# Performance work log

Hardware: AMD Instinct MI355X
Metric: run time of the kernel (lower is better)

## Reference

```python
import jax, jax.numpy as jnp
import numpy as np

KS = 1                      # search radius -> (2*KS+1)^3 = 27 offsets
TEMP = 0.00005              # softmax temperature
COEFS = [0.003, 0.01, 0.03, 0.1, 0.3, 1.0]
H, W, D = 96, 80, 128


def gaussian_kernel3d(channels, sigma=0.5):
    # matches torch GaussianBlur3D: kernel_size = int(2*sigma*2+1) = 3 for sigma=0.5
    ksz = int(2.0 * sigma * 2 + 1)
    c = jnp.arange(ksz, dtype=jnp.float32)
    zz, yy, xx = jnp.meshgrid(c, c, c, indexing='ij')
    mean = (ksz - 1) / 2.0
    var = sigma ** 2
    g = (1.0 / (2.0 * np.pi * var) ** 1.5) * jnp.exp(
        -((zz - mean) ** 2 + (yy - mean) ** 2 + (xx - mean) ** 2) / (2.0 * var))
    g = g / g.sum()
    k = jnp.broadcast_to(g[None, None], (channels, 1, ksz, ksz, ksz))
    return k, ksz // 2


def blur3d(x, kernel, pad):
    # depthwise 3D conv (groups == channels), padding 'same'
    C = x.shape[1]
    return jax.lax.conv_general_dilated(
        x, kernel, window_strides=(1, 1, 1),
        padding=[(pad, pad)] * 3,
        dimension_numbers=('NCDHW', 'OIDHW', 'NCDHW'),
        feature_group_count=C)


def make_offsets(ks):
    n = 2 * ks + 1
    oz, oy, ox = np.meshgrid(np.arange(n) - ks, np.arange(n) - ks,
                             np.arange(n) - ks, indexing='ij')
    off = np.stack([oz.ravel(), oy.ravel(), ox.ravel()], 0).astype(np.float32)
    return jnp.asarray(off).reshape(1, 3, n ** 3, 1, 1, 1)


def cost_volume(src, tgt, ks):
    # -mean_c |src_shifted - tgt| for each of the (2ks+1)^3 offsets
    b, c, h, w, d = src.shape
    xp = jnp.pad(src, ((0, 0), (0, 0), (ks, ks), (ks, ks), (ks, ks)))
    vols = []
    for i in range(2 * ks + 1):
        for j in range(2 * ks + 1):
            for k in range(2 * ks + 1):
                corr = jnp.abs(xp[:, :, i:i + h, j:j + w, k:k + d] - tgt).mean(axis=1)
                vols.append(-corr)
    cv = jnp.stack(vols, axis=1)          # (b, 27, h, w, d)
    return cv[:, None]                    # (b, 1, 27, h, w, d)


def argmax_onehot(cv, temp):
    p = jax.nn.softmax(cv / temp, axis=2)
    return (p == p.max(axis=2, keepdims=True)).astype(cv.dtype)


def setup_inputs() -> dict:
    key = jax.random.key(0)
    k1, k2 = jax.random.split(key)
    source = jax.random.uniform(k1, (1, 1, H, W, D), dtype=jnp.float32)
    target = jax.random.uniform(k2, (1, 1, H, W, D), dtype=jnp.float32)
    return {"source": source, "target": target}


def reference(source, target):
    offsets = make_offsets(KS)                              # (1,3,27,1,1,1)
    n3 = (2 * KS + 1) ** 3
    k_ks, p_ks = gaussian_kernel3d(n3, sigma=0.5)           # 27-ch depthwise blur
    k_3, p_3 = gaussian_kernel3d(3, sigma=0.5)              # 3-ch flow blur

    cv = cost_volume(source, target, KS)                    # (b,1,27,h,w,d)

    cvb = cv[:, 0]
    for _ in range(3):
        cvb = blur3d(cvb, k_ks, p_ks)
    cv = cvb[:, None]

    oh = argmax_onehot(cv, TEMP)                            # (b,1,27,h,w,d)
    flow = (oh * offsets).sum(axis=2)                       # (b,3,h,w,d)
    for _ in range(3):
        flow = blur3d(flow, k_3, p_3)

    for coeff in COEFS:
        # coupling term: squared distance of current flow to each offset
        dist2 = ((flow[:, :, None] - offsets) ** 2).sum(axis=1)  # (b,27,h,w,d)
        coupled = cv - coeff * dist2[:, None]
        oh = argmax_onehot(coupled, TEMP)
        flow = (oh * offsets).sum(axis=2)
        for _ in range(3):
            flow = blur3d(flow, k_3, p_3)
    return flow
```

## Files before the change

### kernel.cpp

```cpp
#include <hip/hip_runtime.h>
#include <math.h>

#define HH 96
#define WW 80
#define DD 128
#define SLICE (WW * DD)
#define NVOX (HH * WW * DD)

struct W4d { double w0, w1, w2, w3; };
struct Raw { float4 t[3]; float4 s[3]; };

__device__ __forceinline__ float4 zf4() { return make_float4(0.f, 0.f, 0.f, 0.f); }

template <bool FUSED>
__global__ __launch_bounds__(256) void blur4_kernel(
    const float* __restrict__ in, const float* __restrict__ src,
    const float* __restrict__ tgt, float* __restrict__ out, int zslab, W4d w) {
  const int tid = threadIdx.x;
  const int lane = tid & 63;
  const int q = lane & 31;
  const int x0 = q << 2;
  const int y = blockIdx.x * 8 + ((tid >> 6) << 1) + (lane >> 5);
  const int c = blockIdx.z;
  const int z0 = blockIdx.y * zslab;
  const int z1 = min(z0 + zslab, HH);

  int oz = 0, oy = 0, ox = 0;
  if (FUSED) { oz = c / 9 - 1; oy = (c / 3) % 3 - 1; ox = c % 3 - 1; }
  const float* __restrict__ inc = FUSED ? (const float*)nullptr : (in + (size_t)c * NVOX);

  auto load_raw = [&](int zz, Raw& r) {
    #pragma unroll
    for (int dy = 0; dy < 3; ++dy) {
      int ry = y - 1 + dy;
      bool rv = ((unsigned)zz < (unsigned)HH) && ((unsigned)ry < (unsigned)WW);
      if (!FUSED) {
        r.t[dy] = rv ? *(const float4*)(inc + (size_t)zz * SLICE + ry * DD + x0) : zf4();
      } else {
        r.t[dy] = rv ? *(const float4*)(tgt + (size_t)zz * SLICE + ry * DD + x0) : zf4();
        int sz = zz + oz, sy = ry + oy;
        bool sv = rv && ((unsigned)sz < (unsigned)HH) && ((unsigned)sy < (unsigned)WW);
        r.s[dy] = sv ? *(const float4*)(src + (size_t)sz * SLICE + sy * DD + x0) : zf4();
      }
    }
  };

  auto finish = [&](const Raw& r, double* P, double* Q) {
    float cc[3][4], cl[3], cr[3];
    #pragma unroll
    for (int dy = 0; dy < 3; ++dy) {
      float4 v;
      if (!FUSED) {
        v = r.t[dy];
      } else {
        float4 s4 = r.s[dy];
        float sl = __shfl_up(s4.w, 1);
        float sr = __shfl_down(s4.x, 1);
        if (q == 0) sl = 0.f;
        if (q == 31) sr = 0.f;
        float4 sh;
        if (ox < 0)      sh = make_float4(sl, s4.x, s4.y, s4.z);
        else if (ox > 0) sh = make_float4(s4.y, s4.z, s4.w, sr);
        else             sh = s4;
        float4 t4 = r.t[dy];
        v.x = -fabsf(__fsub_rn(sh.x, t4.x));
        v.y = -fabsf(__fsub_rn(sh.y, t4.y));
        v.z = -fabsf(__fsub_rn(sh.z, t4.z));
        v.w = -fabsf(__fsub_rn(sh.w, t4.w));
      }
      float l = __shfl_up(v.w, 1);
      float rr = __shfl_down(v.x, 1);
      cc[dy][0] = v.x; cc[dy][1] = v.y; cc[dy][2] = v.z; cc[dy][3] = v.w;
      cl[dy] = (q == 0) ? 0.f : l;
      cr[dy] = (q == 31) ? 0.f : rr;
    }
    auto hs = [&](int row, int i) -> double {
      float a = (i == 0) ? cl[row] : cc[row][i - 1];
      float b = (i == 3) ? cr[row] : cc[row][i + 1];
      return (double)a + (double)b;
    };
    #pragma unroll
    for (int i = 0; i < 4; ++i) {
      double c2 = (double)cc[1][i];
      double f2 = hs(1, i) + ((double)cc[0][i] + (double)cc[2][i]);
      double e2 = hs(0, i) + hs(2, i);
      P[i] = (w.w0 * c2 + w.w1 * f2) + w.w2 * e2;
      Q[i] = (w.w1 * c2 + w.w2 * f2) + w.w3 * e2;
    }
  };

  Raw rA, rB, rC, rD;
  double PA[4], QA[4], PB[4], QB[4], PC[4], QC[4];
  load_raw(z0 - 1, rA);
  load_raw(z0, rB);
  load_raw(z0 + 1, rC);
  finish(rA, PA, QA);
  finish(rB, PB, QB);
  float* ob = out + (size_t)c * NVOX + y * DD + x0;
  for (int z = z0; z < z1; ++z) {
    load_raw(z + 2, rD);
    finish(rC, PC, QC);
    float4 o4;
    o4.x = (float)(PB[0] + (QA[0] + QC[0]));
    o4.y = (float)(PB[1] + (QA[1] + QC[1]));
    o4.z = (float)(PB[2] + (QA[2] + QC[2]));
    o4.w = (float)(PB[3] + (QA[3] + QC[3]));
    *(float4*)(ob + (size_t)z * SLICE) = o4;
    #pragma unroll
    for (int i = 0; i < 4; ++i) {
      PA[i] = PB[i]; QA[i] = QB[i];
      PB[i] = PC[i]; QB[i] = QC[i];
    }
    rC = rD;
  }
}

__global__ __launch_bounds__(256) void flow4_kernel(
    const float* __restrict__ cv, const float* __restrict__ fin,
    float coeff, int couple, float* __restrict__ fout) {
  const int t = blockIdx.x * blockDim.x + threadIdx.x;
  const size_t v = (size_t)t * 4;
  if (v >= (size_t)NVOX) return;
  float4 fz = zf4(), fy = zf4(), fx = zf4();
  if (couple) {
    fz = *(const float4*)(fin + v);
    fy = *(const float4*)(fin + (size_t)NVOX + v);
    fx = *(const float4*)(fin + 2 * (size_t)NVOX + v);
  }
  float best[4] = {-INFINITY, -INFINITY, -INFINITY, -INFINITY};
  float s0[4] = {0, 0, 0, 0}, s1[4] = {0, 0, 0, 0}, s2[4] = {0, 0, 0, 0};
  float fza[4] = {fz.x, fz.y, fz.z, fz.w};
  float fya[4] = {fy.x, fy.y, fy.z, fy.w};
  float fxa[4] = {fx.x, fx.y, fx.z, fx.w};
  #pragma unroll
  for (int o = 0; o < 27; ++o) {
    float4 c4 = *(const float4*)(cv + (size_t)o * NVOX + v);
    const float ozf = (float)(o / 9 - 1);
    const float oyf = (float)((o / 3) % 3 - 1);
    const float oxf = (float)(o % 3 - 1);
    float ca[4] = {c4.x, c4.y, c4.z, c4.w};
    #pragma unroll
    for (int i = 0; i < 4; ++i) {
      float cvv = ca[i];
      if (couple) {
        float dz = __fsub_rn(fza[i], ozf);
        float dy = __fsub_rn(fya[i], oyf);
        float dx = __fsub_rn(fxa[i], oxf);
        float d2 = __fadd_rn(__fadd_rn(__fmul_rn(dz, dz), __fmul_rn(dy, dy)),
                             __fmul_rn(dx, dx));
        cvv = __fsub_rn(cvv, __fmul_rn(coeff, d2));
      }
      float yv = __fdiv_rn(cvv, 5e-5f);
      bool gt = yv > best[i];
      bool eq = yv == best[i];
      best[i] = gt ? yv : best[i];
      s0[i] = gt ? ozf : (eq ? s0[i] + ozf : s0[i]);
      s1[i] = gt ? oyf : (eq ? s1[i] + oyf : s1[i]);
      s2[i] = gt ? oxf : (eq ? s2[i] + oxf : s2[i]);
    }
  }
  *(float4*)(fout + v) = make_float4(s0[0], s0[1], s0[2], s0[3]);
  *(float4*)(fout + (size_t)NVOX + v) = make_float4(s1[0], s1[1], s1[2], s1[3]);
  *(float4*)(fout + 2 * (size_t)NVOX + v) = make_float4(s2[0], s2[1], s2[2], s2[3]);
}

extern "C" void kernel_launch(void* const* d_in, const int* in_sizes, int n_in,
                              void* d_out, int out_size, void* d_ws, size_t ws_size,
                              hipStream_t stream) {
  const float* src = (const float*)d_in[0];
  const float* tgt = (const float*)d_in[1];
  float* out = (float*)d_out;

  float* cv1 = (float*)d_ws;
  float* cv2 = cv1 + (size_t)27 * NVOX;
  float* fa = cv2;
  float* fb = cv2 + (size_t)3 * NVOX;

  float wt[27];
  {
    volatile float factor = (float)(1.0 / pow(2.0 * M_PI * 0.25, 1.5));
    float g[27];
    int o = 0;
    for (int i = 0; i < 3; ++i)
      for (int j = 0; j < 3; ++j)
        for (int k = 0; k < 3; ++k) {
          int d2 = (i - 1) * (i - 1) + (j - 1) * (j - 1) + (k - 1) * (k - 1);
          volatile float e = (float)exp(-2.0 * (double)d2);
          volatile float gg = factor * e;
          g[o++] = gg;
        }
    volatile float r[8];
    for (int j = 0; j < 8; ++j) r[j] = g[j];
    for (int j = 0; j < 8; ++j) r[j] = r[j] + g[8 + j];
    for (int j = 0; j < 8; ++j) r[j] = r[j] + g[16 + j];
    volatile float t01 = r[0] + r[1];
    volatile float t23 = r[2] + r[3];
    volatile float t45 = r[4] + r[5];
    volatile float t67 = r[6] + r[7];
    volatile float h0 = t01 + t23;
    volatile float h1 = t45 + t67;
    volatile float s = h0 + h1;
    s = s + g[24];
    s = s + g[25];
    s = s + g[26];
    for (int t = 0; t < 27; ++t) {
      volatile float w = g[t] / s;
      wt[t] = w;
    }
  }
  W4d wd = {(double)wt[13], (double)wt[12], (double)wt[9], (double)wt[0]};

  dim3 blk(256);
  dim3 gBig(WW / 8, HH / 8, 27);
  dim3 gSm(WW / 8, HH / 3, 3);
  int fblocks = NVOX / 4 / 256;

  blur4_kernel<true><<<gBig, blk, 0, stream>>>(nullptr, src, tgt, cv1, 8, wd);
  blur4_kernel<false><<<gBig, blk, 0, stream>>>(cv1, nullptr, nullptr, cv2, 8, wd);
  blur4_kernel<false><<<gBig, blk, 0, stream>>>(cv2, nullptr, nullptr, cv1, 8, wd);
  flow4_kernel<<<fblocks, blk, 0, stream>>>(cv1, nullptr, 0.f, 0, fa);
  blur4_kernel<false><<<gSm, blk, 0, stream>>>(fa, nullptr, nullptr, fb, 3, wd);
  blur4_kernel<false><<<gSm, blk, 0, stream>>>(fb, nullptr, nullptr, fa, 3, wd);
  blur4_kernel<false><<<gSm, blk, 0, stream>>>(fa, nullptr, nullptr, fb, 3, wd);
  const float coefs[6] = {0.003f, 0.01f, 0.03f, 0.1f, 0.3f, 1.0f};
  for (int it = 0; it < 6; ++it) {
    flow4_kernel<<<fblocks, blk, 0, stream>>>(cv1, fb, coefs[it], 1, fa);
    blur4_kernel<false><<<gSm, blk, 0, stream>>>(fa, nullptr, nullptr, fb, 3, wd);
    blur4_kernel<false><<<gSm, blk, 0, stream>>>(fb, nullptr, nullptr, fa, 3, wd);
    float* dst = (it == 5) ? out : fb;
    blur4_kernel<false><<<gSm, blk, 0, stream>>>(fa, nullptr, nullptr, dst, 3, wd);
  }
}
```

Baseline: 557.8 us.

## Fuse the third flow blur into the coupled argmax kernel and restructure blur math

Folds the last of each group of three flow blurs into a new kernel that blurs the three flow channels for a z-slab in registers and then runs the 27-offset coupled argmax on them. This removes one launch and one write-then-read of the 3-channel flow field per iteration. The blur stencil is refactored to share top and bottom row sums and use fma, which may change double rounding slightly. In exchange, blur work is recomputed at the slab halos and register pressure rises.

```diff
diff --git a/kernel.cpp b/kernel.cpp
--- a/kernel.cpp
+++ b/kernel.cpp
@@ -11,6 +11,54 @@
 struct Raw { float4 t[3]; float4 s[3]; };
 
 __device__ __forceinline__ float4 zf4() { return make_float4(0.f, 0.f, 0.f, 0.f); }
+
+__device__ __forceinline__ void pq_rows(const float4 rows[3], int q, const W4d& w,
+                                        double P[4], double Q[4]) {
+  double d[3][6];
+  #pragma unroll
+  for (int r = 0; r < 3; ++r) {
+    float4 v = rows[r];
+    float l = __shfl_up(v.w, 1);
+    float rr = __shfl_down(v.x, 1);
+    if (q == 0) l = 0.f;
+    if (q == 31) rr = 0.f;
+    d[r][0] = (double)l;
+    d[r][1] = (double)v.x;
+    d[r][2] = (double)v.y;
+    d[r][3] = (double)v.z;
+    d[r][4] = (double)v.w;
+    d[r][5] = (double)rr;
+  }
+  double tb[6];
+  #pragma unroll
+  for (int j = 0; j < 6; ++j) tb[j] = d[0][j] + d[2][j];
+  #pragma unroll
+  for (int i = 0; i < 4; ++i) {
+    double c2 = d[1][i + 1];
+    double f2 = (d[1][i] + d[1][i + 2]) + tb[i + 1];
+    double e2 = tb[i] + tb[i + 2];
+    P[i] = fma(w.w0, c2, fma(w.w1, f2, w.w2 * e2));
+    Q[i] = fma(w.w1, c2, fma(w.w2, f2, w.w3 * e2));
+  }
+}
+
+__device__ __forceinline__ void cv_rows(const Raw& r, int q, int ox, float4 rows[3]) {
+  #pragma unroll
+  for (int dy = 0; dy < 3; ++dy) {
+    float4 s4 = r.s[dy];
+    float sl = __shfl_up(s4.w, 1);
+    float sr = __shfl_down(s4.x, 1);
+    if (q == 0) sl = 0.f;
+    if (q == 31) sr = 0.f;
+    float4 sh;
+    if (ox < 0)      sh = make_float4(sl, s4.x, s4.y, s4.z);
+    else if (ox > 0) sh = make_float4(s4.y, s4.z, s4.w, sr);
+    else             sh = s4;
+    float4 t4 = r.t[dy];
+    rows[dy] = make_float4(-fabsf(__fsub_rn(sh.x, t4.x)), -fabsf(__fsub_rn(sh.y, t4.y)),
+                           -fabsf(__fsub_rn(sh.z, t4.z)), -fabsf(__fsub_rn(sh.w, t4.w)));
+  }
+}
 
 template <bool FUSED>
 __global__ __launch_bounds__(256) void blur4_kernel(
@@ -45,93 +93,121 @@
     }
   };
 
-  auto finish = [&](const Raw& r, double* P, double* Q) {
-    float cc[3][4], cl[3], cr[3];
-    #pragma unroll
-    for (int dy = 0; dy < 3; ++dy) {
-      float4 v;
-      if (!FUSED) {
-        v = r.t[dy];
-      } else {
-        float4 s4 = r.s[dy];
-        float sl = __shfl_up(s4.w, 1);
-        float sr = __shfl_down(s4.x, 1);
-        if (q == 0) sl = 0.f;
-        if (q == 31) sr = 0.f;
-        float4 sh;
-        if (ox < 0)      sh = make_float4(sl, s4.x, s4.y, s4.z);
-        else if (ox > 0) sh = make_float4(s4.y, s4.z, s4.w, sr);
-        else             sh = s4;
-        float4 t4 = r.t[dy];
-        v.x = -fabsf(__fsub_rn(sh.x, t4.x));
-        v.y = -fabsf(__fsub_rn(sh.y, t4.y));
-        v.z = -fabsf(__fsub_rn(sh.z, t4.z));
-        v.w = -fabsf(__fsub_rn(sh.w, t4.w));
-      }
-      float l = __shfl_up(v.w, 1);
-      float rr = __shfl_down(v.x, 1);
-      cc[dy][0] = v.x; cc[dy][1] = v.y; cc[dy][2] = v.z; cc[dy][3] = v.w;
-      cl[dy] = (q == 0) ? 0.f : l;
-      cr[dy] = (q == 31) ? 0.f : rr;
-    }
-    auto hs = [&](int row, int i) -> double {
-      float a = (i == 0) ? cl[row] : cc[row][i - 1];
-      float b = (i == 3) ? cr[row] : cc[row][i + 1];
-      return (double)a + (double)b;
-    };
-    #pragma unroll
-    for (int i = 0; i < 4; ++i) {
-      double c2 = (double)cc[1][i];
-      double f2 = hs(1, i) + ((double)cc[0][i] + (double)cc[2][i]);
-      double e2 = hs(0, i) + hs(2, i);
-      P[i] = (w.w0 * c2 + w.w1 * f2) + w.w2 * e2;
-      Q[i] = (w.w1 * c2 + w.w2 * f2) + w.w3 * e2;
-    }
+  auto finishF = [&](const Raw& r, double P[4], double Q[4]) {
+    float4 rows[3];
+    if (FUSED) cv_rows(r, q, ox, rows);
+    else { rows[0] = r.t[0]; rows[1] = r.t[1]; rows[2] = r.t[2]; }
+    pq_rows(rows, q, w, P, Q);
   };
 
   Raw rA, rB, rC, rD;
-  double PA[4], QA[4], PB[4], QB[4], PC[4], QC[4];
   load_raw(z0 - 1, rA);
   load_raw(z0, rB);
   load_raw(z0 + 1, rC);
-  finish(rA, PA, QA);
-  finish(rB, PB, QB);
+  double Pd[4], Qm[4], Pc[4], Qc[4];
+  finishF(rA, Pd, Qm);
+  finishF(rB, Pc, Qc);
   float* ob = out + (size_t)c * NVOX + y * DD + x0;
   for (int z = z0; z < z1; ++z) {
     load_raw(z + 2, rD);
-    finish(rC, PC, QC);
+    double Pn[4], Qn[4];
+    finishF(rC, Pn, Qn);
     float4 o4;
-    o4.x = (float)(PB[0] + (QA[0] + QC[0]));
-    o4.y = (float)(PB[1] + (QA[1] + QC[1]));
-    o4.z = (float)(PB[2] + (QA[2] + QC[2]));
-    o4.w = (float)(PB[3] + (QA[3] + QC[3]));
+    o4.x = (float)(Pc[0] + (Qm[0] + Qn[0]));
+    o4.y = (float)(Pc[1] + (Qm[1] + Qn[1]));
+    o4.z = (float)(Pc[2] + (Qm[2] + Qn[2]));
+    o4.w = (float)(Pc[3] + (Qm[3] + Qn[3]));
     *(float4*)(ob + (size_t)z * SLICE) = o4;
     #pragma unroll
-    for (int i = 0; i < 4; ++i) {
-      PA[i] = PB[i]; QA[i] = QB[i];
-      PB[i] = PC[i]; QB[i] = QC[i];
-    }
+    for (int i = 0; i < 4; ++i) { Qm[i] = Qc[i]; Qc[i] = Qn[i]; Pc[i] = Pn[i]; }
     rC = rD;
   }
 }
 
+template <int ZSLAB>
+__global__ __launch_bounds__(256) void blur_flow_kernel(
+    const float* __restrict__ fin, const float* __restrict__ cvb,
+    float coeff, float* __restrict__ fout, W4d w) {
+  const int tid = threadIdx.x;
+  const int lane = tid & 63;
+  const int q = lane & 31;
+  const int x0 = q << 2;
+  const int y = blockIdx.x * 8 + ((tid >> 6) << 1) + (lane >> 5);
+  const int z0 = blockIdx.y * ZSLAB;
+
+  float bl[3][ZSLAB][4];
+  #pragma unroll
+  for (int c = 0; c < 3; ++c) {
+    const float* __restrict__ inc = fin + (size_t)c * NVOX;
+    auto load_t = [&](int zz, float4 t3[3]) {
+      #pragma unroll
+      for (int dy = 0; dy < 3; ++dy) {
+        int ry = y - 1 + dy;
+        bool rv = ((unsigned)zz < (unsigned)HH) && ((unsigned)ry < (unsigned)WW);
+        t3[dy] = rv ? *(const float4*)(inc + (size_t)zz * SLICE + ry * DD + x0) : zf4();
+      }
+    };
+    float4 rA[3], rB[3], rC[3], rD[3];
+    load_t(z0 - 1, rA);
+    load_t(z0, rB);
+    load_t(z0 + 1, rC);
+    double Pd[4], Qm[4], Pc[4], Qc[4];
+    pq_rows(rA, q, w, Pd, Qm);
+    pq_rows(rB, q, w, Pc, Qc);
+    #pragma unroll
+    for (int zi = 0; zi < ZSLAB; ++zi) {
+      load_t(z0 + zi + 2, rD);
+      double Pn[4], Qn[4];
+      pq_rows(rC, q, w, Pn, Qn);
+      #pragma unroll
+      for (int i = 0; i < 4; ++i) bl[c][zi][i] = (float)(Pc[i] + (Qm[i] + Qn[i]));
+      #pragma unroll
+      for (int i = 0; i < 4; ++i) { Qm[i] = Qc[i]; Qc[i] = Qn[i]; Pc[i] = Pn[i]; }
+      rC[0] = rD[0]; rC[1] = rD[1]; rC[2] = rD[2];
+    }
+  }
+  #pragma unroll
+  for (int zi = 0; zi < ZSLAB; ++zi) {
+    size_t v = (size_t)(z0 + zi) * SLICE + y * DD + x0;
+    float best[4] = {-INFINITY, -INFINITY, -INFINITY, -INFINITY};
+    float s0[4] = {0, 0, 0, 0}, s1[4] = {0, 0, 0, 0}, s2[4] = {0, 0, 0, 0};
+    #pragma unroll
+    for (int o = 0; o < 27; ++o) {
+      float4 c4 = *(const float4*)(cvb + (size_t)o * NVOX + v);
+      const float ozf = (float)(o / 9 - 1);
+      const float oyf = (float)((o / 3) % 3 - 1);
+      const float oxf = (float)(o % 3 - 1);
+      float ca[4] = {c4.x, c4.y, c4.z, c4.w};
+      #pragma unroll
+      for (int i = 0; i < 4; ++i) {
+        float dz = __fsub_rn(bl[0][zi][i], ozf);
+        float dy2 = __fsub_rn(bl[1][zi][i], oyf);
+        float dx = __fsub_rn(bl[2][zi][i], oxf);
+        float d2 = __fadd_rn(__fadd_rn(__fmul_rn(dz, dz), __fmul_rn(dy2, dy2)),
+                             __fmul_rn(dx, dx));
+        float cvv = __fsub_rn(ca[i], __fmul_rn(coeff, d2));
+        float yv = __fdiv_rn(cvv, 5e-5f);
+        bool gt = yv > best[i];
+        bool eq = yv == best[i];
+        best[i] = gt ? yv : best[i];
+        s0[i] = gt ? ozf : (eq ? s0[i] + ozf : s0[i]);
+        s1[i] = gt ? oyf : (eq ? s1[i] + oyf : s1[i]);
+        s2[i] = gt ? oxf : (eq ? s2[i] + oxf : s2[i]);
+      }
+    }
+    *(float4*)(fout + v) = make_float4(s0[0], s0[1], s0[2], s0[3]);
+    *(float4*)(fout + (size_t)NVOX + v) = make_float4(s1[0], s1[1], s1[2], s1[3]);
+    *(float4*)(fout + 2 * (size_t)NVOX + v) = make_float4(s2[0], s2[1], s2[2], s2[3]);
+  }
+}
+
 __global__ __launch_bounds__(256) void flow4_kernel(
-    const float* __restrict__ cv, const float* __restrict__ fin,
-    float coeff, int couple, float* __restrict__ fout) {
+    const float* __restrict__ cv, float* __restrict__ fout) {
   const int t = blockIdx.x * blockDim.x + threadIdx.x;
   const size_t v = (size_t)t * 4;
   if (v >= (size_t)NVOX) return;
-  float4 fz = zf4(), fy = zf4(), fx = zf4();
-  if (couple) {
-    fz = *(const float4*)(fin + v);
-    fy = *(const float4*)(fin + (size_t)NVOX + v);
-    fx = *(const float4*)(fin + 2 * (size_t)NVOX + v);
-  }
   float best[4] = {-INFINITY, -INFINITY, -INFINITY, -INFINITY};
   float s0[4] = {0, 0, 0, 0}, s1[4] = {0, 0, 0, 0}, s2[4] = {0, 0, 0, 0};
-  float fza[4] = {fz.x, fz.y, fz.z, fz.w};
-  float fya[4] = {fy.x, fy.y, fy.z, fy.w};
-  float fxa[4] = {fx.x, fx.y, fx.z, fx.w};
   #pragma unroll
   for (int o = 0; o < 27; ++o) {
     float4 c4 = *(const float4*)(cv + (size_t)o * NVOX + v);
@@ -141,16 +217,7 @@
     float ca[4] = {c4.x, c4.y, c4.z, c4.w};
     #pragma unroll
     for (int i = 0; i < 4; ++i) {
-      float cvv = ca[i];
-      if (couple) {
-        float dz = __fsub_rn(fza[i], ozf);
-        float dy = __fsub_rn(fya[i], oyf);
-        float dx = __fsub_rn(fxa[i], oxf);
-        float d2 = __fadd_rn(__fadd_rn(__fmul_rn(dz, dz), __fmul_rn(dy, dy)),
-                             __fmul_rn(dx, dx));
-        cvv = __fsub_rn(cvv, __fmul_rn(coeff, d2));
-      }
-      float yv = __fdiv_rn(cvv, 5e-5f);
+      float yv = __fdiv_rn(ca[i], 5e-5f);
       bool gt = yv > best[i];
       bool eq = yv == best[i];
       best[i] = gt ? yv : best[i];
@@ -213,21 +280,28 @@
   dim3 blk(256);
   dim3 gBig(WW / 8, HH / 8, 27);
   dim3 gSm(WW / 8, HH / 3, 3);
+  dim3 gBF(WW / 8, HH / 2);
   int fblocks = NVOX / 4 / 256;
 
   blur4_kernel<true><<<gBig, blk, 0, stream>>>(nullptr, src, tgt, cv1, 8, wd);
   blur4_kernel<false><<<gBig, blk, 0, stream>>>(cv1, nullptr, nullptr, cv2, 8, wd);
   blur4_kernel<false><<<gBig, blk, 0, stream>>>(cv2, nullptr, nullptr, cv1, 8, wd);
-  flow4_kernel<<<fblocks, blk, 0, stream>>>(cv1, nullptr, 0.f, 0, fa);
+  flow4_kernel<<<fblocks, blk, 0, stream>>>(cv1, fa);
   blur4_kernel<false><<<gSm, blk, 0, stream>>>(fa, nullptr, nullptr, fb, 3, wd);
   blur4_kernel<false><<<gSm, blk, 0, stream>>>(fb, nullptr, nullptr, fa, 3, wd);
-  blur4_kernel<false><<<gSm, blk, 0, stream>>>(fa, nullptr, nullptr, fb, 3, wd);
   const float coefs[6] = {0.003f, 0.01f, 0.03f, 0.1f, 0.3f, 1.0f};
+  float* u = fa;
+  float* v = fb;
   for (int it = 0; it < 6; ++it) {
-    flow4_kernel<<<fblocks, blk, 0, stream>>>(cv1, fb, coefs[it], 1, fa);
-    blur4_kernel<false><<<gSm, blk, 0, stream>>>(fa, nullptr, nullptr, fb, 3, wd);
-    blur4_kernel<false><<<gSm, blk, 0, stream>>>(fb, nullptr, nullptr, fa, 3, wd);
-    float* dst = (it == 5) ? out : fb;
-    blur4_kernel<false><<<gSm, blk, 0, stream>>>(fa, nullptr, nullptr, dst, 3, wd);
-  }
-}
+    blur_flow_kernel<2><<<gBF, blk, 0, stream>>>(u, cv1, coefs[it], v, wd);
+    if (it < 5) {
+      blur4_kernel<false><<<gSm, blk, 0, stream>>>(v, nullptr, nullptr, u, 3, wd);
+      blur4_kernel<false><<<gSm, blk, 0, stream>>>(u, nullptr, nullptr, v, 3, wd);
+      float* tswap = u; u = v; v = tswap;
+    } else {
+      blur4_kernel<false><<<gSm, blk, 0, stream>>>(v, nullptr, nullptr, u, 3, wd);
+      blur4_kernel<false><<<gSm, blk, 0, stream>>>(u, nullptr, nullptr, v, 3, wd);
+      blur4_kernel<false><<<gSm, blk, 0, stream>>>(v, nullptr, nullptr, out, 3, wd);
+    }
+  }
+}
```

Result: slower. 829.1 us (+48.6%).

## Restructure blur row math with FMA, narrow flow kernel, shrink z-slabs

Applied to the files above, without the earlier changes.

The blur's separable horizontal/vertical partial sums are rewritten to share top+bottom row sums, use FMA, and keep only the needed P/Q history, which cuts double-precision work and register pressure. The flow argmax kernel now handles 2 voxels per thread instead of 4, doubling thread count for more parallelism. Z-slab sizes shrink (8→6, 3→2) to launch more blocks. Smaller slabs raise halo reload overhead, and FMA may change rounding slightly.

```diff
diff --git a/kernel.cpp b/kernel.cpp
--- a/kernel.cpp
+++ b/kernel.cpp
@@ -11,6 +11,54 @@
 struct Raw { float4 t[3]; float4 s[3]; };
 
 __device__ __forceinline__ float4 zf4() { return make_float4(0.f, 0.f, 0.f, 0.f); }
+
+__device__ __forceinline__ void pq_rows(const float4 rows[3], int q, const W4d& w,
+                                        double P[4], double Q[4]) {
+  double d[3][6];
+  #pragma unroll
+  for (int r = 0; r < 3; ++r) {
+    float4 v = rows[r];
+    float l = __shfl_up(v.w, 1);
+    float rr = __shfl_down(v.x, 1);
+    if (q == 0) l = 0.f;
+    if (q == 31) rr = 0.f;
+    d[r][0] = (double)l;
+    d[r][1] = (double)v.x;
+    d[r][2] = (double)v.y;
+    d[r][3] = (double)v.z;
+    d[r][4] = (double)v.w;
+    d[r][5] = (double)rr;
+  }
+  double tb[6];
+  #pragma unroll
+  for (int j = 0; j < 6; ++j) tb[j] = d[0][j] + d[2][j];
+  #pragma unroll
+  for (int i = 0; i < 4; ++i) {
+    double c2 = d[1][i + 1];
+    double f2 = (d[1][i] + d[1][i + 2]) + tb[i + 1];
+    double e2 = tb[i] + tb[i + 2];
+    P[i] = fma(w.w0, c2, fma(w.w1, f2, w.w2 * e2));
+    Q[i] = fma(w.w1, c2, fma(w.w2, f2, w.w3 * e2));
+  }
+}
+
+__device__ __forceinline__ void cv_rows(const Raw& r, int q, int ox, float4 rows[3]) {
+  #pragma unroll
+  for (int dy = 0; dy < 3; ++dy) {
+    float4 s4 = r.s[dy];
+    float sl = __shfl_up(s4.w, 1);
+    float sr = __shfl_down(s4.x, 1);
+    if (q == 0) sl = 0.f;
+    if (q == 31) sr = 0.f;
+    float4 sh;
+    if (ox < 0)      sh = make_float4(sl, s4.x, s4.y, s4.z);
+    else if (ox > 0) sh = make_float4(s4.y, s4.z, s4.w, sr);
+    else             sh = s4;
+    float4 t4 = r.t[dy];
+    rows[dy] = make_float4(-fabsf(__fsub_rn(sh.x, t4.x)), -fabsf(__fsub_rn(sh.y, t4.y)),
+                           -fabsf(__fsub_rn(sh.z, t4.z)), -fabsf(__fsub_rn(sh.w, t4.w)));
+  }
+}
 
 template <bool FUSED>
 __global__ __launch_bounds__(256) void blur4_kernel(
@@ -45,102 +93,63 @@
     }
   };
 
-  auto finish = [&](const Raw& r, double* P, double* Q) {
-    float cc[3][4], cl[3], cr[3];
-    #pragma unroll
-    for (int dy = 0; dy < 3; ++dy) {
-      float4 v;
-      if (!FUSED) {
-        v = r.t[dy];
-      } else {
-        float4 s4 = r.s[dy];
-        float sl = __shfl_up(s4.w, 1);
-        float sr = __shfl_down(s4.x, 1);
-        if (q == 0) sl = 0.f;
-        if (q == 31) sr = 0.f;
-        float4 sh;
-        if (ox < 0)      sh = make_float4(sl, s4.x, s4.y, s4.z);
-        else if (ox > 0) sh = make_float4(s4.y, s4.z, s4.w, sr);
-        else             sh = s4;
-        float4 t4 = r.t[dy];
-        v.x = -fabsf(__fsub_rn(sh.x, t4.x));
-        v.y = -fabsf(__fsub_rn(sh.y, t4.y));
-        v.z = -fabsf(__fsub_rn(sh.z, t4.z));
-        v.w = -fabsf(__fsub_rn(sh.w, t4.w));
-      }
-      float l = __shfl_up(v.w, 1);
-      float rr = __shfl_down(v.x, 1);
-      cc[dy][0] = v.x; cc[dy][1] = v.y; cc[dy][2] = v.z; cc[dy][3] = v.w;
-      cl[dy] = (q == 0) ? 0.f : l;
-      cr[dy] = (q == 31) ? 0.f : rr;
-    }
-    auto hs = [&](int row, int i) -> double {
-      float a = (i == 0) ? cl[row] : cc[row][i - 1];
-      float b = (i == 3) ? cr[row] : cc[row][i + 1];
-      return (double)a + (double)b;
-    };
-    #pragma unroll
-    for (int i = 0; i < 4; ++i) {
-      double c2 = (double)cc[1][i];
-      double f2 = hs(1, i) + ((double)cc[0][i] + (double)cc[2][i]);
-      double e2 = hs(0, i) + hs(2, i);
-      P[i] = (w.w0 * c2 + w.w1 * f2) + w.w2 * e2;
-      Q[i] = (w.w1 * c2 + w.w2 * f2) + w.w3 * e2;
-    }
+  auto finishF = [&](const Raw& r, double P[4], double Q[4]) {
+    float4 rows[3];
+    if (FUSED) cv_rows(r, q, ox, rows);
+    else { rows[0] = r.t[0]; rows[1] = r.t[1]; rows[2] = r.t[2]; }
+    pq_rows(rows, q, w, P, Q);
   };
 
   Raw rA, rB, rC, rD;
-  double PA[4], QA[4], PB[4], QB[4], PC[4], QC[4];
   load_raw(z0 - 1, rA);
   load_raw(z0, rB);
   load_raw(z0 + 1, rC);
-  finish(rA, PA, QA);
-  finish(rB, PB, QB);
+  double Pd[4], Qm[4], Pc[4], Qc[4];
+  finishF(rA, Pd, Qm);
+  finishF(rB, Pc, Qc);
   float* ob = out + (size_t)c * NVOX + y * DD + x0;
   for (int z = z0; z < z1; ++z) {
     load_raw(z + 2, rD);
-    finish(rC, PC, QC);
+    double Pn[4], Qn[4];
+    finishF(rC, Pn, Qn);
     float4 o4;
-    o4.x = (float)(PB[0] + (QA[0] + QC[0]));
-    o4.y = (float)(PB[1] + (QA[1] + QC[1]));
-    o4.z = (float)(PB[2] + (QA[2] + QC[2]));
-    o4.w = (float)(PB[3] + (QA[3] + QC[3]));
+    o4.x = (float)(Pc[0] + (Qm[0] + Qn[0]));
+    o4.y = (float)(Pc[1] + (Qm[1] + Qn[1]));
+    o4.z = (float)(Pc[2] + (Qm[2] + Qn[2]));
+    o4.w = (float)(Pc[3] + (Qm[3] + Qn[3]));
     *(float4*)(ob + (size_t)z * SLICE) = o4;
     #pragma unroll
-    for (int i = 0; i < 4; ++i) {
-      PA[i] = PB[i]; QA[i] = QB[i];
-      PB[i] = PC[i]; QB[i] = QC[i];
-    }
+    for (int i = 0; i < 4; ++i) { Qm[i] = Qc[i]; Qc[i] = Qn[i]; Pc[i] = Pn[i]; }
     rC = rD;
   }
 }
 
-__global__ __launch_bounds__(256) void flow4_kernel(
+__global__ __launch_bounds__(256) void flow2_kernel(
     const float* __restrict__ cv, const float* __restrict__ fin,
     float coeff, int couple, float* __restrict__ fout) {
   const int t = blockIdx.x * blockDim.x + threadIdx.x;
-  const size_t v = (size_t)t * 4;
+  const size_t v = (size_t)t * 2;
   if (v >= (size_t)NVOX) return;
-  float4 fz = zf4(), fy = zf4(), fx = zf4();
+  float fza[2] = {0.f, 0.f}, fya[2] = {0.f, 0.f}, fxa[2] = {0.f, 0.f};
   if (couple) {
-    fz = *(const float4*)(fin + v);
-    fy = *(const float4*)(fin + (size_t)NVOX + v);
-    fx = *(const float4*)(fin + 2 * (size_t)NVOX + v);
-  }
-  float best[4] = {-INFINITY, -INFINITY, -INFINITY, -INFINITY};
-  float s0[4] = {0, 0, 0, 0}, s1[4] = {0, 0, 0, 0}, s2[4] = {0, 0, 0, 0};
-  float fza[4] = {fz.x, fz.y, fz.z, fz.w};
-  float fya[4] = {fy.x, fy.y, fy.z, fy.w};
-  float fxa[4] = {fx.x, fx.y, fx.z, fx.w};
+    float2 fz = *(const float2*)(fin + v);
+    float2 fy = *(const float2*)(fin + (size_t)NVOX + v);
+    float2 fx = *(const float2*)(fin + 2 * (size_t)NVOX + v);
+    fza[0] = fz.x; fza[1] = fz.y;
+    fya[0] = fy.x; fya[1] = fy.y;
+    fxa[0] = fx.x; fxa[1] = fx.y;
+  }
+  float best[2] = {-INFINITY, -INFINITY};
+  float s0[2] = {0, 0}, s1[2] = {0, 0}, s2[2] = {0, 0};
   #pragma unroll
   for (int o = 0; o < 27; ++o) {
-    float4 c4 = *(const float4*)(cv + (size_t)o * NVOX + v);
+    float2 c2 = *(const float2*)(cv + (size_t)o * NVOX + v);
     const float ozf = (float)(o / 9 - 1);
     const float oyf = (float)((o / 3) % 3 - 1);
     const float oxf = (float)(o % 3 - 1);
-    float ca[4] = {c4.x, c4.y, c4.z, c4.w};
+    float ca[2] = {c2.x, c2.y};
     #pragma unroll
-    for (int i = 0; i < 4; ++i) {
+    for (int i = 0; i < 2; ++i) {
       float cvv = ca[i];
       if (couple) {
         float dz = __fsub_rn(fza[i], ozf);
@@ -159,9 +168,9 @@
       s2[i] = gt ? oxf : (eq ? s2[i] + oxf : s2[i]);
     }
   }
-  *(float4*)(fout + v) = make_float4(s0[0], s0[1], s0[2], s0[3]);
-  *(float4*)(fout + (size_t)NVOX + v) = make_float4(s1[0], s1[1], s1[2], s1[3]);
-  *(float4*)(fout + 2 * (size_t)NVOX + v) = make_float4(s2[0], s2[1], s2[2], s2[3]);
+  *(float2*)(fout + v) = make_float2(s0[0], s0[1]);
+  *(float2*)(fout + (size_t)NVOX + v) = make_float2(s1[0], s1[1]);
+  *(float2*)(fout + 2 * (size_t)NVOX + v) = make_float2(s2[0], s2[1]);
 }
 
 extern "C" void kernel_launch(void* const* d_in, const int* in_sizes, int n_in,
@@ -211,23 +220,23 @@
   W4d wd = {(double)wt[13], (double)wt[12], (double)wt[9], (double)wt[0]};
 
   dim3 blk(256);
-  dim3 gBig(WW / 8, HH / 8, 27);
-  dim3 gSm(WW / 8, HH / 3, 3);
-  int fblocks = NVOX / 4 / 256;
-
-  blur4_kernel<true><<<gBig, blk, 0, stream>>>(nullptr, src, tgt, cv1, 8, wd);
-  blur4_kernel<false><<<gBig, blk, 0, stream>>>(cv1, nullptr, nullptr, cv2, 8, wd);
-  blur4_kernel<false><<<gBig, blk, 0, stream>>>(cv2, nullptr, nullptr, cv1, 8, wd);
-  flow4_kernel<<<fblocks, blk, 0, stream>>>(cv1, nullptr, 0.f, 0, fa);
-  blur4_kernel<false><<<gSm, blk, 0, stream>>>(fa, nullptr, nullptr, fb, 3, wd);
-  blur4_kernel<false><<<gSm, blk, 0, stream>>>(fb, nullptr, nullptr, fa, 3, wd);
-  blur4_kernel<false><<<gSm, blk, 0, stream>>>(fa, nullptr, nullptr, fb, 3, wd);
+  dim3 gBig(WW / 8, HH / 6, 27);
+  dim3 gSm(WW / 8, HH / 2, 3);
+  int fblocks = NVOX / 2 / 256;
+
+  blur4_kernel<true><<<gBig, blk, 0, stream>>>(nullptr, src, tgt, cv1, 6, wd);
+  blur4_kernel<false><<<gBig, blk, 0, stream>>>(cv1, nullptr, nullptr, cv2, 6, wd);
+  blur4_kernel<false><<<gBig, blk, 0, stream>>>(cv2, nullptr, nullptr, cv1, 6, wd);
+  flow2_kernel<<<fblocks, blk, 0, stream>>>(cv1, nullptr, 0.f, 0, fa);
+  blur4_kernel<false><<<gSm, blk, 0, stream>>>(fa, nullptr, nullptr, fb, 2, wd);
+  blur4_kernel<false><<<gSm, blk, 0, stream>>>(fb, nullptr, nullptr, fa, 2, wd);
+  blur4_kernel<false><<<gSm, blk, 0, stream>>>(fa, nullptr, nullptr, fb, 2, wd);
   const float coefs[6] = {0.003f, 0.01f, 0.03f, 0.1f, 0.3f, 1.0f};
   for (int it = 0; it < 6; ++it) {
-    flow4_kernel<<<fblocks, blk, 0, stream>>>(cv1, fb, coefs[it], 1, fa);
-    blur4_kernel<false><<<gSm, blk, 0, stream>>>(fa, nullptr, nullptr, fb, 3, wd);
-    blur4_kernel<false><<<gSm, blk, 0, stream>>>(fb, nullptr, nullptr, fa, 3, wd);
+    flow2_kernel<<<fblocks, blk, 0, stream>>>(cv1, fb, coefs[it], 1, fa);
+    blur4_kernel<false><<<gSm, blk, 0, stream>>>(fa, nullptr, nullptr, fb, 2, wd);
+    blur4_kernel<false><<<gSm, blk, 0, stream>>>(fb, nullptr, nullptr, fa, 2, wd);
     float* dst = (it == 5) ? out : fb;
-    blur4_kernel<false><<<gSm, blk, 0, stream>>>(fa, nullptr, nullptr, dst, 3, wd);
-  }
-}
+    blur4_kernel<false><<<gSm, blk, 0, stream>>>(fa, nullptr, nullptr, dst, 2, wd);
+  }
+}
```

Result: no change. 554.9 us (-0.5%).
